# Kernel optimization log

Measured on AMD Instinct MI355X. Metric: run time of the kernel, lower is better.

Reference implementation:

```python
import jax, jax.numpy as jnp
import numpy as np

N_NODES = 150000  # n_users + m_items
NUM_LAYERS = 3


def setup_inputs() -> dict:
    key = jax.random.key(0)
    k1, k2 = jax.random.split(key)
    x = jax.random.normal(k1, (N_NODES, 64), dtype=jnp.float32) * 0.1
    edge_index = jax.random.randint(k2, (2, 4800000), 0, N_NODES, dtype=jnp.int64)
    return {"x": x, "edge_index": edge_index}


def _lightgcn_propagate(x, row, col, deg_inv_sqrt):
    # message: norm * x[row], aggregated into col (sum)
    norm = deg_inv_sqrt[row] * deg_inv_sqrt[col]  # [E]
    msg = x[row] * norm[:, None]                   # [E, D]
    return jax.ops.segment_sum(msg, col, num_segments=x.shape[0])


def reference(x, edge_index):
    row, col = edge_index[0], edge_index[1]
    # symmetric GCN normalization: deg from destination nodes
    ones = jnp.ones(row.shape, dtype=x.dtype)
    deg = jax.ops.segment_sum(ones, col, num_segments=x.shape[0])
    deg_inv_sqrt = jnp.where(deg > 0, jax.lax.rsqrt(jnp.maximum(deg, 1.0)), 0.0)

    alpha = 1.0 / (1.0 + NUM_LAYERS)
    out = jnp.zeros_like(x)
    h = x
    for _ in range(NUM_LAYERS):
        h = _lightgcn_propagate(h, row, col, deg_inv_sqrt)
        out = out + alpha * h
    return out
```

## Files before the change

### kernel.cpp

```cpp
#include <hip/hip_runtime.h>
#include <hip/hip_fp16.h>
#include <math.h>

#define N_NODES 150000
#define D 64
#define NEDGE 4800000
#define NUM_LAYERS 3

#define BSHIFT 8
#define NBUCKET ((N_NODES + 255) >> 8)
#define NBPAD 768
#define BINTILE 8192
#define NBIN_BLOCKS ((NEDGE + BINTILE - 1) / BINTILE)

__global__ void hist_bucket(const int4* __restrict__ col4, int* __restrict__ bcount) {
    __shared__ int h[NBUCKET];
    for (int i = threadIdx.x; i < NBUCKET; i += blockDim.x) h[i] = 0;
    __syncthreads();
    int i = blockIdx.x * blockDim.x + threadIdx.x;
    int stride = gridDim.x * blockDim.x;
    for (int e = i; e < NEDGE / 4; e += stride) {
        int4 c = col4[e];
        atomicAdd(&h[c.x >> BSHIFT], 1);
        atomicAdd(&h[c.y >> BSHIFT], 1);
        atomicAdd(&h[c.z >> BSHIFT], 1);
        atomicAdd(&h[c.w >> BSHIFT], 1);
    }
    __syncthreads();
    for (int b = threadIdx.x; b < NBUCKET; b += blockDim.x)
        if (h[b]) atomicAdd(&bcount[b], h[b]);
}

__global__ void scan_buckets(const int* __restrict__ bcount, int* __restrict__ bbase,
                             int* __restrict__ bcur16, int* __restrict__ off) {
    __shared__ int tsum[256];
    int t = threadIdx.x;
    int loc[3];
    int s = 0;
#pragma unroll
    for (int k = 0; k < 3; k++) {
        int idx = t * 3 + k;
        int x = (idx < NBUCKET) ? bcount[idx] : 0;
        loc[k] = x;
        s += x;
    }
    tsum[t] = s;
    __syncthreads();
    for (int ofs = 1; ofs < 256; ofs <<= 1) {
        int xv = (t >= ofs) ? tsum[t - ofs] : 0;
        __syncthreads();
        tsum[t] += xv;
        __syncthreads();
    }
    int run = (t > 0) ? tsum[t - 1] : 0;
#pragma unroll
    for (int k = 0; k < 3; k++) {
        int idx = t * 3 + k;
        if (idx < NBUCKET) bbase[idx] = run;
        bcur16[idx * 16] = run;
        run += loc[k];
    }
    if (t == 255) {
        bbase[NBUCKET] = NEDGE;
        off[N_NODES] = NEDGE;
    }
}

__global__ void __launch_bounds__(256) binpass2(const int* __restrict__ row,
                                                const int* __restrict__ col,
                                                int* __restrict__ bcur16,
                                                unsigned* __restrict__ bin) {
    __shared__ unsigned srec[BINTILE];
    __shared__ int hist[NBPAD];
    __shared__ int lscan[NBPAD];
    __shared__ int lcur[NBPAD];
    __shared__ int gbase[NBPAD];
    __shared__ int tsum[256];
    int t = threadIdx.x;
    int base = blockIdx.x * BINTILE;
    int n = NEDGE - base;
    if (n > BINTILE) n = BINTILE;
    for (int i = t; i < NBPAD; i += 256) hist[i] = 0;
    __syncthreads();
    for (int i = t; i < n; i += 256)
        atomicAdd(&hist[col[base + i] >> BSHIFT], 1);
    __syncthreads();
    int b0 = t * 3;
    int l0 = hist[b0], l1 = hist[b0 + 1], l2 = hist[b0 + 2];
    tsum[t] = l0 + l1 + l2;
    __syncthreads();
    for (int ofs = 1; ofs < 256; ofs <<= 1) {
        int xv = (t >= ofs) ? tsum[t - ofs] : 0;
        __syncthreads();
        tsum[t] += xv;
        __syncthreads();
    }
    int run = (t > 0) ? tsum[t - 1] : 0;
    lscan[b0] = run; lcur[b0] = run;
    lscan[b0 + 1] = run + l0; lcur[b0 + 1] = run + l0;
    lscan[b0 + 2] = run + l0 + l1; lcur[b0 + 2] = run + l0 + l1;
    gbase[b0]     = l0 ? atomicAdd(&bcur16[b0 * 16], l0) : 0;
    gbase[b0 + 1] = l1 ? atomicAdd(&bcur16[(b0 + 1) * 16], l1) : 0;
    gbase[b0 + 2] = l2 ? atomicAdd(&bcur16[(b0 + 2) * 16], l2) : 0;
    __syncthreads();
    for (int i = t; i < n; i += 256) {
        int c = col[base + i];
        int r = row[base + i];
        int b = c >> BSHIFT;
        int pos = atomicAdd(&lcur[b], 1);
        srec[pos] = (unsigned)r | ((unsigned)(c & 255) << 18);
    }
    __syncthreads();
#pragma unroll
    for (int k = 0; k < 3; k++) {
        int b = b0 + k;
        int s = lscan[b], e2 = lcur[b], gb = gbase[b];
        for (int j = s; j < e2; j++) bin[gb + (j - s)] = srec[j];
    }
}

__global__ void sortpass2(const unsigned* __restrict__ bin, const int* __restrict__ bbase,
                          float* __restrict__ dis, int* __restrict__ off,
                          unsigned* __restrict__ ewf) {
    __shared__ int hist[256];
    __shared__ int sc[256];
    __shared__ int ncur[256];
    int b = blockIdx.x, t = threadIdx.x;
    int s = bbase[b], e = bbase[b + 1];
    hist[t] = 0;
    __syncthreads();
    for (int i = s + t; i < e; i += 256)
        atomicAdd(&hist[bin[i] >> 18], 1);
    __syncthreads();
    int val = hist[t];
    sc[t] = val;
    __syncthreads();
    for (int ofs = 1; ofs < 256; ofs <<= 1) {
        int xv = (t >= ofs) ? sc[t - ofs] : 0;
        __syncthreads();
        sc[t] += xv;
        __syncthreads();
    }
    int ex = sc[t] - val;
    ncur[t] = ex;
    int node = (b << BSHIFT) + t;
    if (node < N_NODES) {
        dis[node] = (val > 0) ? (1.0f / sqrtf((float)val)) : 0.0f;
        off[node] = s + ex;
    }
    __syncthreads();
    for (int i = s + t; i < e; i += 256) {
        unsigned rec = bin[i];
        int c = (int)(rec >> 18);
        int pos = s + atomicAdd(&ncur[c], 1);
        ewf[pos] = rec & 0x3FFFFu;
    }
}

__global__ void cvt_x(const float4* __restrict__ x4, uint2* __restrict__ xh) {
    int i = blockIdx.x * blockDim.x + threadIdx.x;
    if (i >= N_NODES * 16) return;
    float4 v = x4[i];
    __half2 a = __floats2half2_rn(v.x, v.y);
    __half2 b = __floats2half2_rn(v.z, v.w);
    uint2 r;
    r.x = *reinterpret_cast<unsigned*>(&a);
    r.y = *reinterpret_cast<unsigned*>(&b);
    xh[i] = r;
}

template <bool FINAL>
__global__ void layer8(const uint4* __restrict__ h8, const int* __restrict__ off,
                       const unsigned* __restrict__ ewf, const float* __restrict__ dis,
                       uint4* __restrict__ hout, const uint4* __restrict__ hA,
                       const uint4* __restrict__ hB, float4* __restrict__ out4,
                       float alpha) {
    int wid = (blockIdx.x * blockDim.x + threadIdx.x) >> 6;
    if (wid >= N_NODES) return;
    int lane = threadIdx.x & 63;
    int g = lane >> 3;
    int sub = lane & 7;
    int s = off[wid], e = off[wid + 1];
    float acc[8];
#pragma unroll
    for (int k = 0; k < 8; k++) acc[k] = 0.f;

    auto ACC = [&](uint4 v, float w) {
        const __half2* p = reinterpret_cast<const __half2*>(&v);
#pragma unroll
        for (int k = 0; k < 4; k++) {
            float2 f = __half22float2(p[k]);
            acc[2 * k]     = fmaf(w, f.x, acc[2 * k]);
            acc[2 * k + 1] = fmaf(w, f.y, acc[2 * k + 1]);
        }
    };

    int i = s + g;
    for (; i + 24 < e; i += 32) {
        unsigned r0 = ewf[i], r1 = ewf[i + 8], r2 = ewf[i + 16], r3 = ewf[i + 24];
        float w0 = dis[r0], w1 = dis[r1], w2 = dis[r2], w3 = dis[r3];
        uint4 v0 = h8[(size_t)r0 * 8 + sub];
        uint4 v1 = h8[(size_t)r1 * 8 + sub];
        uint4 v2 = h8[(size_t)r2 * 8 + sub];
        uint4 v3 = h8[(size_t)r3 * 8 + sub];
        ACC(v0, w0); ACC(v1, w1); ACC(v2, w2); ACC(v3, w3);
    }
    for (; i < e; i += 8) {
        unsigned r = ewf[i];
        float w = dis[r];
        uint4 v = h8[(size_t)r * 8 + sub];
        ACC(v, w);
    }
#pragma unroll
    for (int m = 8; m <= 32; m <<= 1)
#pragma unroll
        for (int k = 0; k < 8; k++) acc[k] += __shfl_xor(acc[k], m, 64);

    if (g != 0) return;
    float w = dis[wid];
    if (FINAL) {
        uint4 a = hA[(size_t)wid * 8 + sub];
        uint4 b = hB[(size_t)wid * 8 + sub];
        const __half2* pa = reinterpret_cast<const __half2*>(&a);
        const __half2* pb = reinterpret_cast<const __half2*>(&b);
        float r[8];
#pragma unroll
        for (int k = 0; k < 4; k++) {
            float2 fa = __half22float2(pa[k]);
            float2 fb = __half22float2(pb[k]);
            r[2 * k]     = alpha * (fa.x + fb.x + w * acc[2 * k]);
            r[2 * k + 1] = alpha * (fa.y + fb.y + w * acc[2 * k + 1]);
        }
        out4[(size_t)wid * 16 + sub * 2]     = make_float4(r[0], r[1], r[2], r[3]);
        out4[(size_t)wid * 16 + sub * 2 + 1] = make_float4(r[4], r[5], r[6], r[7]);
    } else {
        __half2 q[4];
#pragma unroll
        for (int k = 0; k < 4; k++)
            q[k] = __floats2half2_rn(w * acc[2 * k], w * acc[2 * k + 1]);
        uint4 st;
        st.x = *reinterpret_cast<unsigned*>(&q[0]);
        st.y = *reinterpret_cast<unsigned*>(&q[1]);
        st.z = *reinterpret_cast<unsigned*>(&q[2]);
        st.w = *reinterpret_cast<unsigned*>(&q[3]);
        hout[(size_t)wid * 8 + sub] = st;
    }
}

extern "C" void kernel_launch(void* const* d_in, const int* in_sizes, int n_in,
                              void* d_out, int out_size, void* d_ws, size_t ws_size,
                              hipStream_t stream) {
    const float* x = (const float*)d_in[0];
    const int* edges = (const int*)d_in[1];
    const int* row = edges;
    const int* col = edges + NEDGE;
    float4* out4 = (float4*)d_out;

    char* ws = (char*)d_ws;
    size_t p = 0;
    auto alloc = [&](size_t bytes) {
        void* r = ws + p;
        p += (bytes + 255) & ~(size_t)255;
        return r;
    };
    int* bcount = (int*)alloc((size_t)NBUCKET * 4);
    int* bbase = (int*)alloc((size_t)(NBUCKET + 1) * 4);
    int* bcur16 = (int*)alloc((size_t)NBPAD * 16 * 4);
    float* dis = (float*)alloc((size_t)N_NODES * 4);
    int* off = (int*)alloc((size_t)(N_NODES + 1) * 4);
    unsigned* ewf = (unsigned*)alloc((size_t)NEDGE * 4);
    uint2* xh = (uint2*)alloc((size_t)N_NODES * D * 2);
    char* region = (char*)alloc((size_t)N_NODES * D * 2);
    unsigned* bin = (unsigned*)region;
    uint4* hA = (uint4*)region;
    uint4* hB = (uint4*)alloc((size_t)N_NODES * D * 2);

    hipMemsetAsync(bcount, 0, (size_t)NBUCKET * 4, stream);
    cvt_x<<<(N_NODES * 16 + 255) / 256, 256, 0, stream>>>((const float4*)x, xh);
    hist_bucket<<<512, 256, 0, stream>>>((const int4*)col, bcount);
    scan_buckets<<<1, 256, 0, stream>>>(bcount, bbase, bcur16, off);
    binpass2<<<NBIN_BLOCKS, 256, 0, stream>>>(row, col, bcur16, bin);
    sortpass2<<<NBUCKET, 256, 0, stream>>>(bin, bbase, dis, off, ewf);

    const float alpha = 1.0f / (1.0f + NUM_LAYERS);
    int grid = (N_NODES * 64 + 255) / 256;
    layer8<false><<<grid, 256, 0, stream>>>((const uint4*)xh, off, ewf, dis,
                                            hA, nullptr, nullptr, nullptr, alpha);
    layer8<false><<<grid, 256, 0, stream>>>((const uint4*)hA, off, ewf, dis,
                                            hB, nullptr, nullptr, nullptr, alpha);
    layer8<true><<<grid, 256, 0, stream>>>((const uint4*)hB, off, ewf, dis,
                                           nullptr, (const uint4*)hA, (const uint4*)hB,
                                           out4, alpha);
}
```

Before: 406.7 us.

## Stage bucket records in LDS and source-ordered scatter; vectorize layer accumulation

sortpass2 now caches each bucket's records in shared memory, so the histogram and the scatter read LDS instead of global memory twice. The scatter runs in five passes split by source-id range, so edges within each destination list come out roughly ordered by source. That ordering is meant to improve gather locality in the layer kernels. The layer kernel also uses 32-bit byte-offset addressing and packed float2 FMAs, aiming to cut address arithmetic and ALU instructions. In exchange, the sort does extra passes and barriers and uses about 36KB of LDS per block, which may reduce occupancy.

```diff
diff --git a/kernel.cpp b/kernel.cpp
--- a/kernel.cpp
+++ b/kernel.cpp
@@ -12,6 +12,9 @@
 #define NBPAD 768
 #define BINTILE 8192
 #define NBIN_BLOCKS ((NEDGE + BINTILE - 1) / BINTILE)
+#define SCAP 9216
+
+typedef float v2f __attribute__((ext_vector_type(2)));
 
 __global__ void hist_bucket(const int4* __restrict__ col4, int* __restrict__ bcount) {
     __shared__ int h[NBUCKET];
@@ -119,18 +122,26 @@
     }
 }
 
-__global__ void sortpass2(const unsigned* __restrict__ bin, const int* __restrict__ bbase,
-                          float* __restrict__ dis, int* __restrict__ off,
-                          unsigned* __restrict__ ewf) {
+__global__ void __launch_bounds__(256) sortpass2(const unsigned* __restrict__ bin,
+                                                 const int* __restrict__ bbase,
+                                                 float* __restrict__ dis,
+                                                 int* __restrict__ off,
+                                                 unsigned* __restrict__ ewf) {
+    __shared__ unsigned srec[SCAP];
     __shared__ int hist[256];
     __shared__ int sc[256];
     __shared__ int ncur[256];
     int b = blockIdx.x, t = threadIdx.x;
     int s = bbase[b], e = bbase[b + 1];
+    int len = e - s;
+    int nst = len < SCAP ? len : SCAP;
+    for (int i = t; i < nst; i += 256) srec[i] = bin[s + i];
     hist[t] = 0;
     __syncthreads();
-    for (int i = s + t; i < e; i += 256)
-        atomicAdd(&hist[bin[i] >> 18], 1);
+    for (int i = t; i < nst; i += 256)
+        atomicAdd(&hist[srec[i] >> 18], 1);
+    for (int i = nst + t; i < len; i += 256)
+        atomicAdd(&hist[bin[s + i] >> 18], 1);
     __syncthreads();
     int val = hist[t];
     sc[t] = val;
@@ -149,8 +160,21 @@
         off[node] = s + ex;
     }
     __syncthreads();
-    for (int i = s + t; i < e; i += 256) {
-        unsigned rec = bin[i];
+#pragma unroll
+    for (int q = 0; q < 5; q++) {
+        for (int i = t; i < nst; i += 256) {
+            unsigned rec = srec[i];
+            unsigned src = rec & 0x3FFFFu;
+            if ((src >> 15) == (unsigned)q) {
+                int c = (int)(rec >> 18);
+                int pos = s + atomicAdd(&ncur[c], 1);
+                ewf[pos] = src;
+            }
+        }
+        __syncthreads();
+    }
+    for (int i = nst + t; i < len; i += 256) {
+        unsigned rec = bin[s + i];
         int c = (int)(rec >> 18);
         int pos = s + atomicAdd(&ncur[c], 1);
         ewf[pos] = rec & 0x3FFFFu;
@@ -170,57 +194,62 @@
 }
 
 template <bool FINAL>
-__global__ void layer8(const uint4* __restrict__ h8, const int* __restrict__ off,
+__global__ void layer8(const char* __restrict__ hbase, const int* __restrict__ off,
                        const unsigned* __restrict__ ewf, const float* __restrict__ dis,
-                       uint4* __restrict__ hout, const uint4* __restrict__ hA,
-                       const uint4* __restrict__ hB, float4* __restrict__ out4,
+                       char* __restrict__ hout, const char* __restrict__ hA,
+                       const char* __restrict__ hB, float4* __restrict__ out4,
                        float alpha) {
     int wid = (blockIdx.x * blockDim.x + threadIdx.x) >> 6;
     if (wid >= N_NODES) return;
-    int lane = threadIdx.x & 63;
-    int g = lane >> 3;
-    int sub = lane & 7;
+    unsigned lane = threadIdx.x & 63u;
+    unsigned g = lane >> 3;
+    unsigned sub16 = (lane & 7u) << 4;
     int s = off[wid], e = off[wid + 1];
-    float acc[8];
-#pragma unroll
-    for (int k = 0; k < 8; k++) acc[k] = 0.f;
+    v2f acc[4];
+#pragma unroll
+    for (int k = 0; k < 4; k++) acc[k] = (v2f){0.f, 0.f};
 
     auto ACC = [&](uint4 v, float w) {
+        v2f wv = {w, w};
         const __half2* p = reinterpret_cast<const __half2*>(&v);
 #pragma unroll
         for (int k = 0; k < 4; k++) {
             float2 f = __half22float2(p[k]);
-            acc[2 * k]     = fmaf(w, f.x, acc[2 * k]);
-            acc[2 * k + 1] = fmaf(w, f.y, acc[2 * k + 1]);
+            v2f fv = {f.x, f.y};
+            acc[k] += fv * wv;
         }
     };
-
-    int i = s + g;
+    auto ROW = [&](unsigned r) {
+        return *reinterpret_cast<const uint4*>(hbase + ((r << 7) | sub16));
+    };
+
+    int i = s + (int)g;
     for (; i + 24 < e; i += 32) {
         unsigned r0 = ewf[i], r1 = ewf[i + 8], r2 = ewf[i + 16], r3 = ewf[i + 24];
         float w0 = dis[r0], w1 = dis[r1], w2 = dis[r2], w3 = dis[r3];
-        uint4 v0 = h8[(size_t)r0 * 8 + sub];
-        uint4 v1 = h8[(size_t)r1 * 8 + sub];
-        uint4 v2 = h8[(size_t)r2 * 8 + sub];
-        uint4 v3 = h8[(size_t)r3 * 8 + sub];
+        uint4 v0 = ROW(r0), v1 = ROW(r1), v2 = ROW(r2), v3 = ROW(r3);
         ACC(v0, w0); ACC(v1, w1); ACC(v2, w2); ACC(v3, w3);
     }
     for (; i < e; i += 8) {
         unsigned r = ewf[i];
         float w = dis[r];
-        uint4 v = h8[(size_t)r * 8 + sub];
+        uint4 v = ROW(r);
         ACC(v, w);
     }
 #pragma unroll
     for (int m = 8; m <= 32; m <<= 1)
 #pragma unroll
-        for (int k = 0; k < 8; k++) acc[k] += __shfl_xor(acc[k], m, 64);
+        for (int k = 0; k < 4; k++) {
+            acc[k].x += __shfl_xor(acc[k].x, m, 64);
+            acc[k].y += __shfl_xor(acc[k].y, m, 64);
+        }
 
     if (g != 0) return;
     float w = dis[wid];
+    unsigned ro = ((unsigned)wid << 7) | sub16;
     if (FINAL) {
-        uint4 a = hA[(size_t)wid * 8 + sub];
-        uint4 b = hB[(size_t)wid * 8 + sub];
+        uint4 a = *reinterpret_cast<const uint4*>(hA + ro);
+        uint4 b = *reinterpret_cast<const uint4*>(hB + ro);
         const __half2* pa = reinterpret_cast<const __half2*>(&a);
         const __half2* pb = reinterpret_cast<const __half2*>(&b);
         float r[8];
@@ -228,22 +257,23 @@
         for (int k = 0; k < 4; k++) {
             float2 fa = __half22float2(pa[k]);
             float2 fb = __half22float2(pb[k]);
-            r[2 * k]     = alpha * (fa.x + fb.x + w * acc[2 * k]);
-            r[2 * k + 1] = alpha * (fa.y + fb.y + w * acc[2 * k + 1]);
+            r[2 * k]     = alpha * (fa.x + fb.x + w * acc[k].x);
+            r[2 * k + 1] = alpha * (fa.y + fb.y + w * acc[k].y);
         }
+        unsigned sub = (lane & 7u);
         out4[(size_t)wid * 16 + sub * 2]     = make_float4(r[0], r[1], r[2], r[3]);
         out4[(size_t)wid * 16 + sub * 2 + 1] = make_float4(r[4], r[5], r[6], r[7]);
     } else {
         __half2 q[4];
 #pragma unroll
         for (int k = 0; k < 4; k++)
-            q[k] = __floats2half2_rn(w * acc[2 * k], w * acc[2 * k + 1]);
+            q[k] = __floats2half2_rn(w * acc[k].x, w * acc[k].y);
         uint4 st;
         st.x = *reinterpret_cast<unsigned*>(&q[0]);
         st.y = *reinterpret_cast<unsigned*>(&q[1]);
         st.z = *reinterpret_cast<unsigned*>(&q[2]);
         st.w = *reinterpret_cast<unsigned*>(&q[3]);
-        hout[(size_t)wid * 8 + sub] = st;
+        *reinterpret_cast<uint4*>(hout + ro) = st;
     }
 }
 
@@ -269,14 +299,14 @@
     float* dis = (float*)alloc((size_t)N_NODES * 4);
     int* off = (int*)alloc((size_t)(N_NODES + 1) * 4);
     unsigned* ewf = (unsigned*)alloc((size_t)NEDGE * 4);
-    uint2* xh = (uint2*)alloc((size_t)N_NODES * D * 2);
+    char* xh = (char*)alloc((size_t)N_NODES * D * 2);
     char* region = (char*)alloc((size_t)N_NODES * D * 2);
     unsigned* bin = (unsigned*)region;
-    uint4* hA = (uint4*)region;
-    uint4* hB = (uint4*)alloc((size_t)N_NODES * D * 2);
+    char* hA = region;
+    char* hB = (char*)alloc((size_t)N_NODES * D * 2);
 
     hipMemsetAsync(bcount, 0, (size_t)NBUCKET * 4, stream);
-    cvt_x<<<(N_NODES * 16 + 255) / 256, 256, 0, stream>>>((const float4*)x, xh);
+    cvt_x<<<(N_NODES * 16 + 255) / 256, 256, 0, stream>>>((const float4*)x, (uint2*)xh);
     hist_bucket<<<512, 256, 0, stream>>>((const int4*)col, bcount);
     scan_buckets<<<1, 256, 0, stream>>>(bcount, bbase, bcur16, off);
     binpass2<<<NBIN_BLOCKS, 256, 0, stream>>>(row, col, bcur16, bin);
@@ -284,11 +314,10 @@
 
     const float alpha = 1.0f / (1.0f + NUM_LAYERS);
     int grid = (N_NODES * 64 + 255) / 256;
-    layer8<false><<<grid, 256, 0, stream>>>((const uint4*)xh, off, ewf, dis,
+    layer8<false><<<grid, 256, 0, stream>>>(xh, off, ewf, dis,
                                             hA, nullptr, nullptr, nullptr, alpha);
-    layer8<false><<<grid, 256, 0, stream>>>((const uint4*)hA, off, ewf, dis,
+    layer8<false><<<grid, 256, 0, stream>>>(hA, off, ewf, dis,
                                             hB, nullptr, nullptr, nullptr, alpha);
-    layer8<true><<<grid, 256, 0, stream>>>((const uint4*)hB, off, ewf, dis,
-                                           nullptr, (const uint4*)hA, (const uint4*)hB,
-                                           out4, alpha);
-}
+    layer8<true><<<grid, 256, 0, stream>>>(hB, off, ewf, dis,
+                                           nullptr, hA, hB, out4, alpha);
+}
```

New measurement: 407.7 us. No clear change (+0.2%).
